# Kernel optimization log

Measured on AMD Instinct MI355X. Metric: run time of the kernel, lower is better.

The kernel has to match this reference:

```python
import jax, jax.numpy as jnp
import numpy as np
import math

B, NP, PL, CIN = 32, 1024, 16, 8
C = PL * CIN          # channels = 128
D = 512               # d_model
H = 8                 # n_heads
DH = D // H           # 64
DFF = 2048
E, TOPK = 4, 2
M = int(DH * math.log(DH))  # 266 performer random features


def _ortho_proj(m, d, rng):
    # gaussian-orthogonal random features, rows rescaled by gaussian norms (FAVOR+, scaling=0)
    blocks = []
    for _ in range(m // d + 1):
        q, _ = np.linalg.qr(rng.normal(size=(d, d)))
        blocks.append(q.T)
    mat = np.concatenate(blocks, 0)[:m]
    mult = np.linalg.norm(rng.normal(size=(m, d)), axis=1)
    return jnp.asarray((mat * mult[:, None]).astype(np.float32))


def setup_inputs() -> dict:
    key = jax.random.key(0)
    ks = jax.random.split(key, 16)
    rng = np.random.default_rng(0)
    s = lambda k, sh, fan: (jax.random.normal(k, sh, jnp.float32) / np.sqrt(fan))
    return {
        "x": jax.random.normal(ks[0], (B, NP, PL, CIN), jnp.float32),
        "emb_w": s(ks[1], (D, C), C),
        "wq": s(ks[2], (D, D), D), "bq": jnp.zeros((D,), jnp.float32),
        "wk": s(ks[3], (D, D), D), "bk": jnp.zeros((D,), jnp.float32),
        "wv": s(ks[4], (D, D), D), "bv": jnp.zeros((D,), jnp.float32),
        "wo": s(ks[5], (D, D), D), "bo": jnp.zeros((D,), jnp.float32),
        "proj": _ortho_proj(M, DH, rng),
        "ln2_g": jnp.ones((D,), jnp.float32), "ln2_b": jnp.zeros((D,), jnp.float32),
        "ln3_g": jnp.ones((D,), jnp.float32), "ln3_b": jnp.zeros((D,), jnp.float32),
        "gate_w": s(ks[6], (E, D), D), "gate_b": jnp.zeros((E,), jnp.float32),
        "w1": s(ks[7], (E, D, DFF), D), "b1": jnp.zeros((E, DFF), jnp.float32),
        "w2": s(ks[8], (E, DFF, D), DFF), "b2": jnp.zeros((E, D), jnp.float32),
    }


def _ln(x, g, b):
    mu = jnp.mean(x, -1, keepdims=True)
    var = jnp.var(x, -1, keepdims=True)
    return (x - mu) / jnp.sqrt(var + 1e-5) * g + b


def _phi(data, proj, is_query):
    # FAVOR+ softmax kernel feature map
    dh = data.shape[-1]
    m = proj.shape[0]
    dn = dh ** -0.25
    dash = jnp.einsum('...nd,md->...nm', data * dn, proj)
    diag = jnp.sum(jnp.square(data), -1, keepdims=True) * (0.5 * dn * dn)
    stab = jnp.max(dash, -1, keepdims=True) if is_query else jnp.max(dash)
    return (m ** -0.5) * (jnp.exp(dash - diag - stab) + 1e-4)


def reference(x, emb_w, wq, bq, wk, bk, wv, bv, wo, bo, proj,
              ln2_g, ln2_b, ln3_g, ln3_b, gate_w, gate_b, w1, b1, w2, b2):
    b, n = x.shape[0], x.shape[1]
    xe = x.reshape(b, n, -1) @ emb_w.T          # [b, n, D] (bias-free embedding)
    xe = xe[:, None]                            # [b, 1, n, D]
    # ---- Performer self-attention ----
    heads = lambda t: t.reshape(b, 1, n, H, DH).transpose(0, 1, 3, 2, 4)  # [b,1,h,n,dh]
    q = heads(xe @ wq.T + bq)
    k = heads(xe @ wk.T + bk)
    v = heads(xe @ wv.T + bv)
    qp = _phi(q, proj, True)                    # [b,1,h,n,m]
    kp = _phi(k, proj, False)
    ctx = jnp.einsum('...nm,...nd->...md', kp, v)           # [b,1,h,m,dh]
    den = jnp.einsum('...nm,...m->...n', qp, kp.sum(-2))    # [b,1,h,n]
    attn = jnp.einsum('...nm,...md->...nd', qp, ctx) / den[..., None]
    attn = attn.transpose(0, 1, 3, 2, 4).reshape(b, 1, n, D) @ wo.T + bo
    h1 = _ln(xe + attn, ln2_g, ln2_b)
    # ---- SparseMoE feed-forward (top-2 of 4 experts) ----
    t = h1.reshape(-1, D)                       # [T, D], T = b*n
    logits = t @ gate_w.T + gate_b              # [T, E]
    topv, topi = jax.lax.top_k(logits, TOPK)
    gwt = jax.nn.softmax(topv, -1)              # softmax over selected experts
    wfull = (jax.nn.one_hot(topi, E, dtype=t.dtype) * gwt[..., None]).sum(1)  # [T, E]
    hmid = jax.nn.relu(jnp.einsum('td,edf->etf', t, w1) + b1[:, None])        # [E, T, DFF]
    y = jnp.einsum('etf,efd->etd', hmid, w2) + b2[:, None]                    # [E, T, D]
    moe = jnp.einsum('te,etd->td', wfull, y).reshape(b, 1, n, D)
    return _ln(h1 + moe, ln3_g, ln3_b)          # dropout = identity in eval
```

## Files before the change

### kernel.cpp

```cpp
#include <hip/hip_runtime.h>
#include <math.h>

#define NBATCH 32
#define NPOS   1024
#define NTOK   32768
#define DMODEL 512
#define NHEAD  8
#define DHD    64
#define NROWS  262144
#define MMR    266
#define NDFF   2048
#define NEXP   4
#define CIN    128

#define DNSC   0.35355339059327373f
#define RSM    0.06131393394849658f
#define NEG_INF -3.0e38f

typedef _Float16 half8 __attribute__((ext_vector_type(8)));
typedef _Float16 half4 __attribute__((ext_vector_type(4)));
typedef float    f32x4 __attribute__((ext_vector_type(4)));

static const size_t F_BUF1 = 0;
static const size_t F_CTX  = 16777216;
static const size_t F_KSUM = 21135360;
static const size_t F_PART = 21203456;
static const size_t F_STAB = 21205504;
static const size_t F_EFF  = 21205520;
static const size_t F_CNTI = 21402128;
static const size_t F_TOKI = 21402144;
static const size_t F_GWF  = 21533216;
static const size_t F_PJT  = 21664288;
static const size_t F_END  = 21684768;

#define DASH17(da, q) \
  da[0]+=q*pA.x; da[1]+=q*pA.y; da[2]+=q*pA.z; da[3]+=q*pA.w; \
  da[4]+=q*pB.x; da[5]+=q*pB.y; da[6]+=q*pB.z; da[7]+=q*pB.w; \
  da[8]+=q*pC.x; da[9]+=q*pC.y; da[10]+=q*pC.z; da[11]+=q*pC.w; \
  da[12]+=q*pD.x; da[13]+=q*pD.y; da[14]+=q*pD.z; da[15]+=q*pD.w; \
  da[16]+=q*pE;

__global__ __launch_bounds__(256) void fallback_zero_kernel(float* __restrict__ out) {
  out[(size_t)blockIdx.x * 256 + threadIdx.x] = 0.f;
}

__global__ __launch_bounds__(256) void proj_pack_kernel(
    const float* __restrict__ proj, float* __restrict__ projT)
{
  int idx = blockIdx.x * 256 + threadIdx.x;
  if (idx >= 20480) return;
  int d = idx / 320, rem = idx % 320;
  int g = rem / 20, j = rem % 20;
  int m = g * 17 + j;
  projT[idx] = (j < 17 && m < MMR) ? proj[m * 64 + d] : 0.f;
}

__global__ __launch_bounds__(128) void effmat_kernel(
    const float* __restrict__ wq, const float* __restrict__ wk, const float* __restrict__ wv,
    const float* __restrict__ emb, float* __restrict__ eff)
{
  __shared__ float wrow[512];
  const int bid = blockIdx.x;
  const int mat = bid >> 9;
  const int n   = bid & 511;
  const float* W = (mat == 0) ? wq : ((mat == 1) ? wk : wv);
  const int tid = threadIdx.x;
  for (int i = tid; i < 512; i += 128) wrow[i] = W[n * 512 + i];
  __syncthreads();
  float acc = 0.f;
  for (int d = 0; d < 512; ++d) acc += wrow[d] * emb[d * CIN + tid];
  eff[mat * 65536 + n * CIN + tid] = acc;
}

__global__ __launch_bounds__(256) void gemm_nt_kernel(
    const float* __restrict__ A, const float* __restrict__ W, int K,
    const float* __restrict__ A2, const float* __restrict__ W2, int K2,
    const float* __restrict__ bias, float* __restrict__ C, int N, int ncb)
{
  __shared__ float As[32][64];
  __shared__ float Ws[32][64];
  const int tid  = threadIdx.x;
  const int bx   = blockIdx.x % ncb;
  const int by   = blockIdx.x / ncb;
  const int row0 = by * 64, col0 = bx * 64;
  const int tx   = tid & 15, ty = tid >> 4;
  const int lr   = tid >> 3;
  const int lk   = (tid & 7) * 4;
  float acc[4][4] = {};
  for (int pass = 0; pass < 2; ++pass) {
    const float* Ap = pass ? A2 : A;
    const float* Wp = pass ? W2 : W;
    const int    Kp = pass ? K2 : K;
    if (!Ap) continue;
    for (int k0 = 0; k0 < Kp; k0 += 32) {
      __syncthreads();
#pragma unroll
      for (int rr = 0; rr < 2; ++rr) {
        const int r = lr + rr * 32;
        float4 a4 = *(const float4*)&Ap[(size_t)(row0 + r) * Kp + k0 + lk];
        As[lk + 0][r] = a4.x; As[lk + 1][r] = a4.y; As[lk + 2][r] = a4.z; As[lk + 3][r] = a4.w;
        float4 w4 = *(const float4*)&Wp[(size_t)(col0 + r) * Kp + k0 + lk];
        Ws[lk + 0][r] = w4.x; Ws[lk + 1][r] = w4.y; Ws[lk + 2][r] = w4.z; Ws[lk + 3][r] = w4.w;
      }
      __syncthreads();
#pragma unroll
      for (int kk = 0; kk < 32; ++kk) {
        float4 av = *(const float4*)&As[kk][ty * 4];
        float4 wv = *(const float4*)&Ws[kk][tx * 4];
        acc[0][0] += av.x * wv.x; acc[0][1] += av.x * wv.y; acc[0][2] += av.x * wv.z; acc[0][3] += av.x * wv.w;
        acc[1][0] += av.y * wv.x; acc[1][1] += av.y * wv.y; acc[1][2] += av.y * wv.z; acc[1][3] += av.y * wv.w;
        acc[2][0] += av.z * wv.x; acc[2][1] += av.z * wv.y; acc[2][2] += av.z * wv.z; acc[2][3] += av.z * wv.w;
        acc[3][0] += av.w * wv.x; acc[3][1] += av.w * wv.y; acc[3][2] += av.w * wv.z; acc[3][3] += av.w * wv.w;
      }
    }
  }
#pragma unroll
  for (int i = 0; i < 4; ++i) {
    const int row = row0 + ty * 4 + i;
    const int col = col0 + tx * 4;
    float4 o = make_float4(acc[i][0], acc[i][1], acc[i][2], acc[i][3]);
    if (bias) {
      float4 b4 = *(const float4*)&bias[col];
      o.x += b4.x; o.y += b4.y; o.z += b4.z; o.w += b4.w;
    }
    *(float4*)&C[(size_t)row * N + col] = o;
  }
}

__global__ __launch_bounds__(1024) void kdash_max_kernel(
    const float* __restrict__ Kbuf, const float* __restrict__ projT, float* __restrict__ partial)
{
  __shared__ float pjG[20480];
  __shared__ float kl[32 * 68];
  __shared__ float red[1024];
  const int tid = threadIdx.x;
  for (int i = tid; i < 20480; i += 1024) pjG[i] = projT[i];
  const int w = tid >> 6, l = tid & 63;
  const int ml = l & 15, ds = l >> 4;
  const int dbase = ds * 16;
  const int r0 = 2 * w;
  float mxl = NEG_INF;
  for (int t = 0; t < 16; ++t) {
    __syncthreads();
    for (int idx = tid; idx < 2048; idx += 1024) {
      int r = idx >> 6, dd = idx & 63;
      kl[r * 68 + dd] = Kbuf[((size_t)blockIdx.x * 512 + t * 32 + r) * 64 + dd] * DNSC;
    }
    __syncthreads();
    float da0[17], da1[17];
#pragma unroll
    for (int j = 0; j < 17; ++j) { da0[j] = 0.f; da1[j] = 0.f; }
    for (int dd = 0; dd < 16; ++dd) {
      int d = dbase + dd;
      float q0 = kl[r0 * 68 + d], q1 = kl[r0 * 68 + 68 + d];
      const float* pr = &pjG[d * 320 + ml * 20];
      float4 pA = *(const float4*)pr, pB = *(const float4*)(pr + 4),
             pC = *(const float4*)(pr + 8), pD = *(const float4*)(pr + 12);
      float pE = pr[16];
      DASH17(da0, q0)
      DASH17(da1, q1)
    }
#pragma unroll
    for (int j = 0; j < 17; ++j) {
      da0[j] += __shfl_xor(da0[j], 16); da0[j] += __shfl_xor(da0[j], 32);
      da1[j] += __shfl_xor(da1[j], 16); da1[j] += __shfl_xor(da1[j], 32);
    }
#pragma unroll
    for (int j = 0; j < 17; ++j) {
      int m = ml * 17 + j;
      if (m < MMR) { mxl = fmaxf(mxl, da0[j]); mxl = fmaxf(mxl, da1[j]); }
    }
  }
  red[tid] = mxl;
  __syncthreads();
  for (int st = 512; st > 0; st >>= 1) {
    if (tid < st) red[tid] = fmaxf(red[tid], red[tid + st]);
    __syncthreads();
  }
  if (tid == 0) partial[blockIdx.x] = red[0];
}

__global__ __launch_bounds__(256) void reduce_max_kernel(
    const float* __restrict__ part, float* __restrict__ stab, int n)
{
  __shared__ float red[256];
  float m = NEG_INF;
  for (int i = threadIdx.x; i < n; i += 256) m = fmaxf(m, part[i]);
  red[threadIdx.x] = m;
  __syncthreads();
  for (int st = 128; st > 0; st >>= 1) {
    if (threadIdx.x < st) red[threadIdx.x] = fmaxf(red[threadIdx.x], red[threadIdx.x + st]);
    __syncthreads();
  }
  if (threadIdx.x == 0) stab[0] = red[0];
}

__global__ __launch_bounds__(1024) void ctx_kernel(
    const float* __restrict__ Kbuf, const float* __restrict__ Vbuf,
    const float* __restrict__ projT, const float* __restrict__ stabp,
    float* __restrict__ ctxg, float* __restrict__ ksumg)
{
  __shared__ float pjG[20480];
  __shared__ float kl[32 * 68];
  __shared__ float vl[32 * 68];
  __shared__ _Float16 kp16[32 * 320];
  __shared__ float ks[272];
  const int tid = threadIdx.x;
  const int bh = blockIdx.x;
  const int b = bh >> 3, h = bh & 7;
  const float stab = stabp[0];
  for (int i = tid; i < 20480; i += 1024) pjG[i] = projT[i];
  if (tid < 272) ks[tid] = 0.f;
  const int w = tid >> 6, l = tid & 63;
  const int ml = l & 15, ds = l >> 4;
  const int dbase = ds * 16;
  const int r0 = 2 * w;
  const int jh = ds >> 1, rsel = ds & 1;
  const int d = tid & 63, mg = tid >> 6;
  const int ksm = tid >> 1, ksih = tid & 1;
  const int ksg = ksm / 17, ksj = ksm - ksg * 17;
  float acc[17];
#pragma unroll
  for (int j = 0; j < 17; ++j) acc[j] = 0.f;

  for (int t = 0; t < 32; ++t) {
    __syncthreads();
    for (int idx = tid; idx < 2048; idx += 1024) {
      int r = idx >> 6, dd = idx & 63;
      size_t g = ((size_t)(b * NPOS + t * 32 + r)) * DMODEL + h * DHD + dd;
      kl[r * 68 + dd] = Kbuf[g] * DNSC;
      vl[r * 68 + dd] = Vbuf[g];
    }
    __syncthreads();
    float da0[17], da1[17]; float dg0 = 0.f, dg1 = 0.f;
#pragma unroll
    for (int j = 0; j < 17; ++j) { da0[j] = 0.f; da1[j] = 0.f; }
    for (int dd = 0; dd < 16; ++dd) {
      int dq = dbase + dd;
      float q0 = kl[r0 * 68 + dq], q1 = kl[r0 * 68 + 68 + dq];
      const float* pr = &pjG[dq * 320 + ml * 20];
      float4 pA = *(const float4*)pr, pB = *(const float4*)(pr + 4),
             pC = *(const float4*)(pr + 8), pD = *(const float4*)(pr + 12);
      float pE = pr[16];
      dg0 += q0 * q0; dg1 += q1 * q1;
      DASH17(da0, q0)
      DASH17(da1, q1)
    }
#pragma unroll
    for (int j = 0; j < 17; ++j) {
      da0[j] += __shfl_xor(da0[j], 16); da0[j] += __shfl_xor(da0[j], 32);
      da1[j] += __shfl_xor(da1[j], 16); da1[j] += __shfl_xor(da1[j], 32);
    }
    dg0 += __shfl_xor(dg0, 16); dg0 += __shfl_xor(dg0, 32);
    dg1 += __shfl_xor(dg1, 16); dg1 += __shfl_xor(dg1, 32);
    float dgx = rsel ? dg1 : dg0;
    const int irow = r0 + rsel;
#pragma unroll
    for (int k = 0; k < 9; ++k) {
      int j = 2 * k + jh;
      if (j < 17) {
        int m = ml * 17 + j;
        float dv = rsel ? da1[j] : da0[j];
        float v = 0.f;
        if (m < MMR) v = RSM * (expf(dv - 0.5f * dgx - stab) + 1e-4f);
        kp16[irow * 320 + ml * 20 + j] = (_Float16)v;
      }
    }
    __syncthreads();
    if (tid < 544) {
      float s = 0.f;
      const _Float16* kb = &kp16[ksih * 16 * 320 + ksg * 20 + ksj];
#pragma unroll
      for (int i = 0; i < 16; ++i) s += (float)kb[i * 320];
      s += __shfl_xor(s, 1);
      if (ksih == 0) ks[ksm] += s;
    }
    for (int i = 0; i < 32; ++i) {
      float vv = vl[i * 68 + d];
      const _Float16* kr = &kp16[i * 320 + mg * 20];
      half4 k0 = *(const half4*)kr;
      half4 k1 = *(const half4*)(kr + 4);
      half4 k2 = *(const half4*)(kr + 8);
      half4 k3 = *(const half4*)(kr + 12);
      float kE = (float)kr[16];
      acc[0] += (float)k0.x * vv; acc[1] += (float)k0.y * vv; acc[2] += (float)k0.z * vv; acc[3] += (float)k0.w * vv;
      acc[4] += (float)k1.x * vv; acc[5] += (float)k1.y * vv; acc[6] += (float)k1.z * vv; acc[7] += (float)k1.w * vv;
      acc[8] += (float)k2.x * vv; acc[9] += (float)k2.y * vv; acc[10] += (float)k2.z * vv; acc[11] += (float)k2.w * vv;
      acc[12] += (float)k3.x * vv; acc[13] += (float)k3.y * vv; acc[14] += (float)k3.z * vv; acc[15] += (float)k3.w * vv;
      acc[16] += kE * vv;
    }
  }
  __syncthreads();
  const size_t cb = (size_t)bh * MMR * DHD;
#pragma unroll
  for (int j = 0; j < 17; ++j) {
    int m = mg * 17 + j;
    if (m < MMR) ctxg[cb + (size_t)m * 64 + d] = acc[j];
  }
  if (tid < MMR) ksumg[bh * MMR + tid] = ks[tid];
}

__global__ __launch_bounds__(1024) void attn_kernel(
    const float* __restrict__ Qbuf, const float* __restrict__ ctxg,
    const float* __restrict__ ksumg, const float* __restrict__ projT,
    float* __restrict__ attnb)
{
  __shared__ float pjG[20480];
  __shared__ float ql[64 * 68];
  __shared__ _Float16 qp16[64 * 272];
  __shared__ float ks[272];
  __shared__ float den_s[64];
  const int tid = threadIdx.x;
  const int bh = blockIdx.x >> 4;
  const int n0 = (blockIdx.x & 15) * 64;
  const int b = bh >> 3, h = bh & 7;
  for (int i = tid; i < 20480; i += 1024) pjG[i] = projT[i];
  if (tid < 272) ks[tid] = (tid < MMR) ? ksumg[bh * MMR + tid] : 0.f;
  for (int idx = tid; idx < 4096; idx += 1024) {
    int r = idx >> 6, dd = idx & 63;
    ql[r * 68 + dd] = Qbuf[((size_t)(b * NPOS + n0 + r)) * DMODEL + h * DHD + dd] * DNSC;
  }
  __syncthreads();
  const int w = tid >> 6, l = tid & 63;
  const int ml = l & 15, ds = l >> 4;
  const int dbase = ds * 16;
  const int jh = ds >> 1, rsel = ds & 1;
  for (int s = 0; s < 2; ++s) {
    const int r0 = s * 32 + 2 * w;
    float da0[17], da1[17]; float dg0 = 0.f, dg1 = 0.f;
#pragma unroll
    for (int j = 0; j < 17; ++j) { da0[j] = 0.f; da1[j] = 0.f; }
    for (int dd = 0; dd < 16; ++dd) {
      int dq = dbase + dd;
      float q0 = ql[r0 * 68 + dq], q1 = ql[r0 * 68 + 68 + dq];
      const float* pr = &pjG[dq * 320 + ml * 20];
      float4 pA = *(const float4*)pr, pB = *(const float4*)(pr + 4),
             pC = *(const float4*)(pr + 8), pD = *(const float4*)(pr + 12);
      float pE = pr[16];
      dg0 += q0 * q0; dg1 += q1 * q1;
      DASH17(da0, q0)
      DASH17(da1, q1)
    }
#pragma unroll
    for (int j = 0; j < 17; ++j) {
      da0[j] += __shfl_xor(da0[j], 16); da0[j] += __shfl_xor(da0[j], 32);
      da1[j] += __shfl_xor(da1[j], 16); da1[j] += __shfl_xor(da1[j], 32);
    }
    dg0 += __shfl_xor(dg0, 16); dg0 += __shfl_xor(dg0, 32);
    dg1 += __shfl_xor(dg1, 16); dg1 += __shfl_xor(dg1, 32);
    float mx0 = NEG_INF, mx1 = NEG_INF;
#pragma unroll
    for (int j = 0; j < 17; ++j) {
      int m = ml * 17 + j;
      if (m < MMR) { mx0 = fmaxf(mx0, da0[j]); mx1 = fmaxf(mx1, da1[j]); }
    }
#pragma unroll
    for (int off = 1; off < 16; off <<= 1) {
      mx0 = fmaxf(mx0, __shfl_xor(mx0, off));
      mx1 = fmaxf(mx1, __shfl_xor(mx1, off));
    }
    float dgx = rsel ? dg1 : dg0;
    float mxx = rsel ? mx1 : mx0;
    const int row = r0 + rsel;
    float dp = 0.f;
#pragma unroll
    for (int k = 0; k < 9; ++k) {
      int j = 2 * k + jh;
      if (j < 17) {
        int m = ml * 17 + j;
        float dv = rsel ? da1[j] : da0[j];
        float v = 0.f;
        if (m < MMR) { v = RSM * (expf(dv - 0.5f * dgx - mxx) + 1e-4f); dp += v * ks[m]; }
        qp16[row * 272 + m] = (_Float16)v;
      }
    }
    dp += __shfl_xor(dp, 1); dp += __shfl_xor(dp, 2); dp += __shfl_xor(dp, 4);
    dp += __shfl_xor(dp, 8); dp += __shfl_xor(dp, 32);
    if ((l & 47) == 0) den_s[row] = dp;
  }
  __syncthreads();
  const int wg = tid >> 6, lane = tid & 63;
  float acc[4] = {0.f, 0.f, 0.f, 0.f};
  const float* cb = ctxg + (size_t)bh * MMR * DHD + lane;
  for (int m0 = 0; m0 < 272; m0 += 4) {
    float c0 = cb[(size_t)(m0 + 0) * 64];
    float c1 = cb[(size_t)(m0 + 1) * 64];
    float c2 = cb[(size_t)(m0 + 2) * 64];
    float c3 = cb[(size_t)(m0 + 3) * 64];
#pragma unroll
    for (int tt = 0; tt < 4; ++tt) {
      half4 q4 = *(const half4*)&qp16[(wg * 4 + tt) * 272 + m0];
      acc[tt] += (float)q4.x * c0 + (float)q4.y * c1 + (float)q4.z * c2 + (float)q4.w * c3;
    }
  }
#pragma unroll
  for (int tt = 0; tt < 4; ++tt) {
    int r = wg * 4 + tt;
    attnb[((size_t)(b * NPOS + n0 + r)) * DMODEL + h * DHD + lane] = acc[tt] / den_s[r];
  }
}

__global__ __launch_bounds__(256) void ln_kernel(
    const float* __restrict__ in, const float* __restrict__ g, const float* __restrict__ bb,
    float* __restrict__ out, float* __restrict__ out2)
{
  const int row = blockIdx.x, tid = threadIdx.x;
  float2 x = *(const float2*)&in[(size_t)row * DMODEL + tid * 2];
  float s = x.x + x.y, sq = x.x * x.x + x.y * x.y;
#pragma unroll
  for (int off = 32; off > 0; off >>= 1) {
    s += __shfl_down(s, off);
    sq += __shfl_down(sq, off);
  }
  __shared__ float ps[4], pq[4];
  __shared__ float smu, srv;
  const int wv = tid >> 6, ln = tid & 63;
  if (ln == 0) { ps[wv] = s; pq[wv] = sq; }
  __syncthreads();
  if (tid == 0) {
    float S = ps[0] + ps[1] + ps[2] + ps[3];
    float Q = pq[0] + pq[1] + pq[2] + pq[3];
    float mu = S / 512.f;
    float var = Q / 512.f - mu * mu;
    smu = mu;
    srv = 1.0f / sqrtf(var + 1e-5f);
  }
  __syncthreads();
  const float mu = smu, rv = srv;
  const int c = tid * 2;
  float y0 = (x.x - mu) * rv * g[c] + bb[c];
  float y1 = (x.y - mu) * rv * g[c + 1] + bb[c + 1];
  out[(size_t)row * DMODEL + c] = y0;
  out[(size_t)row * DMODEL + c + 1] = y1;
  if (out2) {
    out2[(size_t)row * DMODEL + c] = y0;
    out2[(size_t)row * DMODEL + c + 1] = y1;
  }
}

__global__ __launch_bounds__(64) void zero_cnt_kernel(int* __restrict__ cnt)
{
  if (threadIdx.x < NEXP) cnt[threadIdx.x] = 0;
}

__global__ __launch_bounds__(256) void gate_kernel(
    const float* __restrict__ h1, const float* __restrict__ gw, const float* __restrict__ gb,
    int* __restrict__ cnt, int* __restrict__ toks, float* __restrict__ gws)
{
  const int wv = threadIdx.x >> 6, ln = threadIdx.x & 63;
  const int tok = blockIdx.x * 4 + wv;
  const float* hr = h1 + (size_t)tok * DMODEL;
  float p0 = 0, p1 = 0, p2 = 0, p3 = 0;
#pragma unroll
  for (int k = 0; k < 8; ++k) {
    float xv = hr[ln + 64 * k];
    p0 += xv * gw[0 * DMODEL + ln + 64 * k];
    p1 += xv * gw[1 * DMODEL + ln + 64 * k];
    p2 += xv * gw[2 * DMODEL + ln + 64 * k];
    p3 += xv * gw[3 * DMODEL + ln + 64 * k];
  }
#pragma unroll
  for (int off = 32; off > 0; off >>= 1) {
    p0 += __shfl_down(p0, off);
    p1 += __shfl_down(p1, off);
    p2 += __shfl_down(p2, off);
    p3 += __shfl_down(p3, off);
  }
  if (ln == 0) {
    p0 += gb[0]; p1 += gb[1]; p2 += gb[2]; p3 += gb[3];
    int i0 = 0; float v0 = p0;
    if (p1 > v0) { v0 = p1; i0 = 1; }
    if (p2 > v0) { v0 = p2; i0 = 2; }
    if (p3 > v0) { v0 = p3; i0 = 3; }
    int i1 = -1; float v1 = NEG_INF;
    if (i0 != 0 && p0 > v1) { v1 = p0; i1 = 0; }
    if (i0 != 1 && p1 > v1) { v1 = p1; i1 = 1; }
    if (i0 != 2 && p2 > v1) { v1 = p2; i1 = 2; }
    if (i0 != 3 && p3 > v1) { v1 = p3; i1 = 3; }
    float e = expf(v1 - v0);
    float w0 = 1.f / (1.f + e);
    float w1 = e / (1.f + e);
    int pos0 = atomicAdd(&cnt[i0], 1);
    toks[i0 * NTOK + pos0] = tok;
    gws[i0 * NTOK + pos0] = w0;
    int pos1 = atomicAdd(&cnt[i1], 1);
    toks[i1 * NTOK + pos1] = tok;
    gws[i1 * NTOK + pos1] = w1;
  }
}

__global__ __launch_bounds__(256) void transpose_f16_kernel(
    const float* __restrict__ in, _Float16* __restrict__ outp, int R, int C)
{
  __shared__ float tl[32][33];
  const int bid = blockIdx.x;
  const int e  = bid >> 10;
  const int t2 = bid & 1023;
  const int tC = C >> 5;
  const int r0 = (t2 / tC) << 5;
  const int c0 = (t2 % tC) << 5;
  const float* ine  = in   + (size_t)e * R * C;
  _Float16*    oute = outp + (size_t)e * R * C;
  const int ci = threadIdx.x & 31, ri = threadIdx.x >> 5;
#pragma unroll
  for (int i = 0; i < 4; ++i)
    tl[ri + i * 8][ci] = ine[(size_t)(r0 + ri + i * 8) * C + c0 + ci];
  __syncthreads();
  const int rr = threadIdx.x & 31, cc = threadIdx.x >> 5;
#pragma unroll
  for (int i = 0; i < 4; ++i)
    oute[(size_t)(c0 + cc + i * 8) * R + r0 + rr] = (_Float16)tl[rr][cc + i * 8];
}

__global__ __launch_bounds__(512) void moe_mfma_kernel(
    const float* __restrict__ h1, const _Float16* __restrict__ w1t, const float* __restrict__ b1,
    const _Float16* __restrict__ w2t, const float* __restrict__ b2,
    const int* __restrict__ cnt, const int* __restrict__ toks, const float* __restrict__ gws,
    float* __restrict__ Z)
{
  __shared__ _Float16 t_lds[64 * 520];
  __shared__ _Float16 hm[64 * 264];
  __shared__ int   tk_s[64];
  __shared__ float gw_s[64];
  const int tid = threadIdx.x;
  const int e = blockIdx.x >> 10;
  const int tile = blockIdx.x & 1023;
  const int cn = cnt[e];
  if (tile * 64 >= cn) return;
  if (tid < 64) {
    int idx = tile * 64 + tid;
    if (idx < cn) { tk_s[tid] = toks[e * NTOK + idx]; gw_s[tid] = gws[e * NTOK + idx]; }
    else          { tk_s[tid] = -1;                   gw_s[tid] = 0.f; }
  }
  __syncthreads();
  for (int it = tid; it < 64 * 128; it += 512) {
    int r = it >> 7, c4 = (it & 127) * 4;
    int tk = tk_s[r];
    float4 v = make_float4(0.f, 0.f, 0.f, 0.f);
    if (tk >= 0) v = *(const float4*)&h1[(size_t)tk * DMODEL + c4];
    _Float16* p = &t_lds[r * 520 + c4];
    p[0] = (_Float16)v.x; p[1] = (_Float16)v.y; p[2] = (_Float16)v.z; p[3] = (_Float16)v.w;
  }
  __syncthreads();

  const int w = tid >> 6, l = tid & 63;
  const int lr = l & 15, lg = l >> 4;
  const _Float16* w1e = w1t + (size_t)e * NDFF * DMODEL;
  const _Float16* w2e = w2t + (size_t)e * DMODEL * NDFF;
  const float* b1e = b1 + e * NDFF;

  f32x4 acc2[4][4];
#pragma unroll
  for (int mt = 0; mt < 4; ++mt)
#pragma unroll
    for (int nt = 0; nt < 4; ++nt) acc2[mt][nt] = (f32x4){0.f, 0.f, 0.f, 0.f};

  for (int fc = 0; fc < 8; ++fc) {
    f32x4 acc1[4][2];
#pragma unroll
    for (int mt = 0; mt < 4; ++mt)
#pragma unroll
      for (int nt1 = 0; nt1 < 2; ++nt1) acc1[mt][nt1] = (f32x4){0.f, 0.f, 0.f, 0.f};
#pragma unroll
    for (int ks = 0; ks < 16; ++ks) {
      half8 am[4];
#pragma unroll
      for (int mt = 0; mt < 4; ++mt)
        am[mt] = *(const half8*)&t_lds[(mt * 16 + lr) * 520 + ks * 32 + lg * 8];
#pragma unroll
      for (int nt1 = 0; nt1 < 2; ++nt1) {
        half8 bfr = *(const half8*)&w1e[(size_t)(fc * 256 + w * 32 + nt1 * 16 + lr) * DMODEL + ks * 32 + lg * 8];
#pragma unroll
        for (int mt = 0; mt < 4; ++mt)
          acc1[mt][nt1] = __builtin_amdgcn_mfma_f32_16x16x32_f16(am[mt], bfr, acc1[mt][nt1], 0, 0, 0);
      }
    }
#pragma unroll
    for (int nt1 = 0; nt1 < 2; ++nt1) {
      float b1v = b1e[fc * 256 + w * 32 + nt1 * 16 + lr];
#pragma unroll
      for (int mt = 0; mt < 4; ++mt)
#pragma unroll
        for (int r = 0; r < 4; ++r)
          hm[(mt * 16 + lg * 4 + r) * 264 + w * 32 + nt1 * 16 + lr] =
              (_Float16)fmaxf(acc1[mt][nt1][r] + b1v, 0.f);
    }
    __syncthreads();
#pragma unroll
    for (int ks2 = 0; ks2 < 8; ++ks2) {
      half8 am[4];
#pragma unroll
      for (int mt = 0; mt < 4; ++mt)
        am[mt] = *(const half8*)&hm[(mt * 16 + lr) * 264 + ks2 * 32 + lg * 8];
#pragma unroll
      for (int nt = 0; nt < 4; ++nt) {
        half8 bfr = *(const half8*)&w2e[(size_t)(w * 64 + nt * 16 + lr) * NDFF + fc * 256 + ks2 * 32 + lg * 8];
#pragma unroll
        for (int mt = 0; mt < 4; ++mt)
          acc2[mt][nt] = __builtin_amdgcn_mfma_f32_16x16x32_f16(am[mt], bfr, acc2[mt][nt], 0, 0, 0);
      }
    }
    __syncthreads();
  }

  const float* b2e = b2 + e * DMODEL;
#pragma unroll
  for (int nt = 0; nt < 4; ++nt) {
    float b2v = b2e[w * 64 + nt * 16 + lr];
#pragma unroll
    for (int mt = 0; mt < 4; ++mt) {
#pragma unroll
      for (int r = 0; r < 4; ++r) {
        int row = mt * 16 + lg * 4 + r;
        int tk = tk_s[row];
        if (tk >= 0)
          atomicAdd(&Z[(size_t)tk * DMODEL + w * 64 + nt * 16 + lr],
                    (acc2[mt][nt][r] + b2v) * gw_s[row]);
      }
    }
  }
}

extern "C" void kernel_launch(void* const* d_in, const int* in_sizes, int n_in,
                              void* d_out, int out_size, void* d_ws, size_t ws_size,
                              hipStream_t stream) {
  const float* x     = (const float*)d_in[0];
  const float* emb_w = (const float*)d_in[1];
  const float* wq    = (const float*)d_in[2];
  const float* bq    = (const float*)d_in[3];
  const float* wk    = (const float*)d_in[4];
  const float* bk    = (const float*)d_in[5];
  const float* wv    = (const float*)d_in[6];
  const float* bv    = (const float*)d_in[7];
  const float* wo    = (const float*)d_in[8];
  const float* bo    = (const float*)d_in[9];
  const float* proj  = (const float*)d_in[10];
  const float* ln2g  = (const float*)d_in[11];
  const float* ln2b  = (const float*)d_in[12];
  const float* ln3g  = (const float*)d_in[13];
  const float* ln3b  = (const float*)d_in[14];
  const float* gatew = (const float*)d_in[15];
  const float* gateb = (const float*)d_in[16];
  const float* w1    = (const float*)d_in[17];
  const float* b1    = (const float*)d_in[18];
  const float* w2    = (const float*)d_in[19];
  const float* b2    = (const float*)d_in[20];
  float* out = (float*)d_out;
  float* ws  = (float*)d_ws;

  if (ws_size < F_END * sizeof(float)) {
    fallback_zero_kernel<<<NTOK * 2, 256, 0, stream>>>(out);
    return;
  }

  float* BUF1 = ws + F_BUF1;
  float* BUF2 = out;
  int*   cnt  = (int*)(ws + F_CNTI);
  int*   toks = (int*)(ws + F_TOKI);
  float* gwf  = ws + F_GWF;
  _Float16* w1t = (_Float16*)(ws + F_CTX);
  _Float16* w2t = w1t + (size_t)NEXP * NDFF * DMODEL;

  zero_cnt_kernel<<<1, 64, 0, stream>>>(cnt);
  proj_pack_kernel<<<80, 256, 0, stream>>>(proj, ws + F_PJT);
  effmat_kernel<<<1536, 128, 0, stream>>>(wq, wk, wv, emb_w, ws + F_EFF);
  gemm_nt_kernel<<<4096, 256, 0, stream>>>(x, ws + F_EFF + 65536, CIN, nullptr, nullptr, 0, bk, BUF1, DMODEL, 8);
  gemm_nt_kernel<<<4096, 256, 0, stream>>>(x, ws + F_EFF + 131072, CIN, nullptr, nullptr, 0, bv, BUF2, DMODEL, 8);
  kdash_max_kernel<<<512, 1024, 0, stream>>>(BUF1, ws + F_PJT, ws + F_PART);
  reduce_max_kernel<<<1, 256, 0, stream>>>(ws + F_PART, ws + F_STAB, 512);
  ctx_kernel<<<256, 1024, 0, stream>>>(BUF1, BUF2, ws + F_PJT, ws + F_STAB, ws + F_CTX, ws + F_KSUM);
  gemm_nt_kernel<<<4096, 256, 0, stream>>>(x, ws + F_EFF, CIN, nullptr, nullptr, 0, bq, BUF1, DMODEL, 8);
  attn_kernel<<<4096, 1024, 0, stream>>>(BUF1, ws + F_CTX, ws + F_KSUM, ws + F_PJT, BUF2);
  transpose_f16_kernel<<<4096, 256, 0, stream>>>(w1, w1t, DMODEL, NDFF);
  transpose_f16_kernel<<<4096, 256, 0, stream>>>(w2, w2t, NDFF, DMODEL);
  gemm_nt_kernel<<<4096, 256, 0, stream>>>(BUF2, wo, DMODEL, x, emb_w, CIN, bo, BUF1, DMODEL, 8);
  ln_kernel<<<NTOK, 256, 0, stream>>>(BUF1, ln2g, ln2b, BUF2, BUF1);
  gate_kernel<<<8192, 256, 0, stream>>>(BUF2, gatew, gateb, cnt, toks, gwf);
  moe_mfma_kernel<<<4096, 512, 0, stream>>>(BUF2, w1t, b1, w2t, b2, cnt, toks, gwf, BUF1);
  ln_kernel<<<NTOK, 256, 0, stream>>>(BUF1, ln3g, ln3b, out, nullptr);
}
```

Baseline: 5.262 ms.

## Halve block size of performer attention kernels to fit two blocks per CU

The kdash_max, ctx and attn kernels drop from 1024 to 512 threads per block and declare two blocks per CU. Per-step row tiles are halved, and the shared-memory feature layout is padded to 32-half strides so each thread can read features with 16-byte vector loads. ctx_kernel now has each thread accumulate two feature groups, and attn_kernel runs twice as many blocks over 32-row tiles. The aim is better occupancy and fewer barrier stalls, but the 80KB projection table is still copied into shared memory in every block, which may limit residency and doubles that copy in attn.

Result: faster. 4.643 ms (-11.8%).

```diff
diff --git a/kernel.cpp b/kernel.cpp
--- a/kernel.cpp
+++ b/kernel.cpp
@@ -7,7 +7,6 @@
 #define DMODEL 512
 #define NHEAD  8
 #define DHD    64
-#define NROWS  262144
 #define MMR    266
 #define NDFF   2048
 #define NEXP   4
@@ -127,24 +126,25 @@
   }
 }
 
-__global__ __launch_bounds__(1024) void kdash_max_kernel(
+__global__ __launch_bounds__(512, 2) void kdash_max_kernel(
     const float* __restrict__ Kbuf, const float* __restrict__ projT, float* __restrict__ partial)
 {
   __shared__ float pjG[20480];
-  __shared__ float kl[32 * 68];
-  __shared__ float red[1024];
+  __shared__ float kl[16 * 68];
+  __shared__ float red[512];
   const int tid = threadIdx.x;
-  for (int i = tid; i < 20480; i += 1024) pjG[i] = projT[i];
+  for (int i4 = tid; i4 < 5120; i4 += 512)
+    ((float4*)pjG)[i4] = ((const float4*)projT)[i4];
   const int w = tid >> 6, l = tid & 63;
   const int ml = l & 15, ds = l >> 4;
   const int dbase = ds * 16;
   const int r0 = 2 * w;
   float mxl = NEG_INF;
-  for (int t = 0; t < 16; ++t) {
-    __syncthreads();
-    for (int idx = tid; idx < 2048; idx += 1024) {
+  for (int t = 0; t < 32; ++t) {
+    __syncthreads();
+    for (int idx = tid; idx < 1024; idx += 512) {
       int r = idx >> 6, dd = idx & 63;
-      kl[r * 68 + dd] = Kbuf[((size_t)blockIdx.x * 512 + t * 32 + r) * 64 + dd] * DNSC;
+      kl[r * 68 + dd] = Kbuf[((size_t)blockIdx.x * 512 + t * 16 + r) * 64 + dd] * DNSC;
     }
     __syncthreads();
     float da0[17], da1[17];
@@ -173,7 +173,7 @@
   }
   red[tid] = mxl;
   __syncthreads();
-  for (int st = 512; st > 0; st >>= 1) {
+  for (int st = 256; st > 0; st >>= 1) {
     if (tid < st) red[tid] = fmaxf(red[tid], red[tid + st]);
     __syncthreads();
   }
@@ -195,41 +195,43 @@
   if (threadIdx.x == 0) stab[0] = red[0];
 }
 
-__global__ __launch_bounds__(1024) void ctx_kernel(
+__global__ __launch_bounds__(512, 2) void ctx_kernel(
     const float* __restrict__ Kbuf, const float* __restrict__ Vbuf,
     const float* __restrict__ projT, const float* __restrict__ stabp,
     float* __restrict__ ctxg, float* __restrict__ ksumg)
 {
   __shared__ float pjG[20480];
-  __shared__ float kl[32 * 68];
-  __shared__ float vl[32 * 68];
-  __shared__ _Float16 kp16[32 * 320];
+  __shared__ float kl[16 * 68];
+  __shared__ float vl[16 * 68];
+  __shared__ _Float16 kp16[16 * 512];
   __shared__ float ks[272];
   const int tid = threadIdx.x;
   const int bh = blockIdx.x;
   const int b = bh >> 3, h = bh & 7;
   const float stab = stabp[0];
-  for (int i = tid; i < 20480; i += 1024) pjG[i] = projT[i];
+  for (int i4 = tid; i4 < 5120; i4 += 512)
+    ((float4*)pjG)[i4] = ((const float4*)projT)[i4];
   if (tid < 272) ks[tid] = 0.f;
   const int w = tid >> 6, l = tid & 63;
   const int ml = l & 15, ds = l >> 4;
   const int dbase = ds * 16;
   const int r0 = 2 * w;
   const int jh = ds >> 1, rsel = ds & 1;
-  const int d = tid & 63, mg = tid >> 6;
-  const int ksm = tid >> 1, ksih = tid & 1;
-  const int ksg = ksm / 17, ksj = ksm - ksg * 17;
-  float acc[17];
-#pragma unroll
-  for (int j = 0; j < 17; ++j) acc[j] = 0.f;
-
-  for (int t = 0; t < 32; ++t) {
-    __syncthreads();
-    for (int idx = tid; idx < 2048; idx += 1024) {
+  const int d = l;
+  const int ksg = tid / 17, ksj = tid - ksg * 17;
+  float acc[2][17];
+#pragma unroll
+  for (int g = 0; g < 2; ++g)
+#pragma unroll
+    for (int j = 0; j < 17; ++j) acc[g][j] = 0.f;
+
+  for (int t = 0; t < 64; ++t) {
+    __syncthreads();
+    for (int idx = tid; idx < 1024; idx += 512) {
       int r = idx >> 6, dd = idx & 63;
-      size_t g = ((size_t)(b * NPOS + t * 32 + r)) * DMODEL + h * DHD + dd;
-      kl[r * 68 + dd] = Kbuf[g] * DNSC;
-      vl[r * 68 + dd] = Vbuf[g];
+      size_t gg = ((size_t)(b * NPOS + t * 16 + r)) * DMODEL + h * DHD + dd;
+      kl[r * 68 + dd] = Kbuf[gg] * DNSC;
+      vl[r * 68 + dd] = Vbuf[gg];
     }
     __syncthreads();
     float da0[17], da1[17]; float dg0 = 0.f, dg1 = 0.f;
@@ -263,60 +265,66 @@
         float dv = rsel ? da1[j] : da0[j];
         float v = 0.f;
         if (m < MMR) v = RSM * (expf(dv - 0.5f * dgx - stab) + 1e-4f);
-        kp16[irow * 320 + ml * 20 + j] = (_Float16)v;
-      }
-    }
-    __syncthreads();
-    if (tid < 544) {
+        kp16[irow * 512 + ml * 32 + j] = (_Float16)v;
+      }
+    }
+    __syncthreads();
+    if (tid < 272) {
       float s = 0.f;
-      const _Float16* kb = &kp16[ksih * 16 * 320 + ksg * 20 + ksj];
-#pragma unroll
-      for (int i = 0; i < 16; ++i) s += (float)kb[i * 320];
-      s += __shfl_xor(s, 1);
-      if (ksih == 0) ks[ksm] += s;
-    }
-    for (int i = 0; i < 32; ++i) {
+      const _Float16* kb = &kp16[ksg * 32 + ksj];
+#pragma unroll
+      for (int i = 0; i < 16; ++i) s += (float)kb[i * 512];
+      ks[tid] += s;
+    }
+    for (int i = 0; i < 16; ++i) {
       float vv = vl[i * 68 + d];
-      const _Float16* kr = &kp16[i * 320 + mg * 20];
-      half4 k0 = *(const half4*)kr;
-      half4 k1 = *(const half4*)(kr + 4);
-      half4 k2 = *(const half4*)(kr + 8);
-      half4 k3 = *(const half4*)(kr + 12);
-      float kE = (float)kr[16];
-      acc[0] += (float)k0.x * vv; acc[1] += (float)k0.y * vv; acc[2] += (float)k0.z * vv; acc[3] += (float)k0.w * vv;
-      acc[4] += (float)k1.x * vv; acc[5] += (float)k1.y * vv; acc[6] += (float)k1.z * vv; acc[7] += (float)k1.w * vv;
-      acc[8] += (float)k2.x * vv; acc[9] += (float)k2.y * vv; acc[10] += (float)k2.z * vv; acc[11] += (float)k2.w * vv;
-      acc[12] += (float)k3.x * vv; acc[13] += (float)k3.y * vv; acc[14] += (float)k3.z * vv; acc[15] += (float)k3.w * vv;
-      acc[16] += kE * vv;
-    }
-  }
-  __syncthreads();
+#pragma unroll
+      for (int g = 0; g < 2; ++g) {
+        const _Float16* kr = &kp16[i * 512 + (2 * w + g) * 32];
+        half8 kA = *(const half8*)kr;
+        half8 kB = *(const half8*)(kr + 8);
+        float kE = (float)kr[16];
+        acc[g][0] += (float)kA[0] * vv; acc[g][1] += (float)kA[1] * vv;
+        acc[g][2] += (float)kA[2] * vv; acc[g][3] += (float)kA[3] * vv;
+        acc[g][4] += (float)kA[4] * vv; acc[g][5] += (float)kA[5] * vv;
+        acc[g][6] += (float)kA[6] * vv; acc[g][7] += (float)kA[7] * vv;
+        acc[g][8] += (float)kB[0] * vv; acc[g][9] += (float)kB[1] * vv;
+        acc[g][10] += (float)kB[2] * vv; acc[g][11] += (float)kB[3] * vv;
+        acc[g][12] += (float)kB[4] * vv; acc[g][13] += (float)kB[5] * vv;
+        acc[g][14] += (float)kB[6] * vv; acc[g][15] += (float)kB[7] * vv;
+        acc[g][16] += kE * vv;
+      }
+    }
+  }
   const size_t cb = (size_t)bh * MMR * DHD;
 #pragma unroll
-  for (int j = 0; j < 17; ++j) {
-    int m = mg * 17 + j;
-    if (m < MMR) ctxg[cb + (size_t)m * 64 + d] = acc[j];
-  }
+  for (int g = 0; g < 2; ++g)
+#pragma unroll
+    for (int j = 0; j < 17; ++j) {
+      int m = (2 * w + g) * 17 + j;
+      if (m < MMR) ctxg[cb + (size_t)m * 64 + d] = acc[g][j];
+    }
   if (tid < MMR) ksumg[bh * MMR + tid] = ks[tid];
 }
 
-__global__ __launch_bounds__(1024) void attn_kernel(
+__global__ __launch_bounds__(512, 2) void attn_kernel(
     const float* __restrict__ Qbuf, const float* __restrict__ ctxg,
     const float* __restrict__ ksumg, const float* __restrict__ projT,
     float* __restrict__ attnb)
 {
   __shared__ float pjG[20480];
-  __shared__ float ql[64 * 68];
-  __shared__ _Float16 qp16[64 * 272];
+  __shared__ float ql[32 * 68];
+  __shared__ _Float16 qp16[32 * 512];
   __shared__ float ks[272];
-  __shared__ float den_s[64];
+  __shared__ float den_s[32];
   const int tid = threadIdx.x;
-  const int bh = blockIdx.x >> 4;
-  const int n0 = (blockIdx.x & 15) * 64;
+  const int bh = blockIdx.x >> 5;
+  const int n0 = (blockIdx.x & 31) * 32;
   const int b = bh >> 3, h = bh & 7;
-  for (int i = tid; i < 20480; i += 1024) pjG[i] = projT[i];
+  for (int i4 = tid; i4 < 5120; i4 += 512)
+    ((float4*)pjG)[i4] = ((const float4*)projT)[i4];
   if (tid < 272) ks[tid] = (tid < MMR) ? ksumg[bh * MMR + tid] : 0.f;
-  for (int idx = tid; idx < 4096; idx += 1024) {
+  for (int idx = tid; idx < 2048; idx += 512) {
     int r = idx >> 6, dd = idx & 63;
     ql[r * 68 + dd] = Qbuf[((size_t)(b * NPOS + n0 + r)) * DMODEL + h * DHD + dd] * DNSC;
   }
@@ -326,7 +334,7 @@
   const int dbase = ds * 16;
   const int jh = ds >> 1, rsel = ds & 1;
   for (int s = 0; s < 2; ++s) {
-    const int r0 = s * 32 + 2 * w;
+    const int r0 = s * 16 + 2 * w;
     float da0[17], da1[17]; float dg0 = 0.f, dg1 = 0.f;
 #pragma unroll
     for (int j = 0; j < 17; ++j) { da0[j] = 0.f; da1[j] = 0.f; }
@@ -371,7 +379,7 @@
         float dv = rsel ? da1[j] : da0[j];
         float v = 0.f;
         if (m < MMR) { v = RSM * (expf(dv - 0.5f * dgx - mxx) + 1e-4f); dp += v * ks[m]; }
-        qp16[row * 272 + m] = (_Float16)v;
+        qp16[row * 512 + ml * 32 + j] = (_Float16)v;
       }
     }
     dp += __shfl_xor(dp, 1); dp += __shfl_xor(dp, 2); dp += __shfl_xor(dp, 4);
@@ -382,15 +390,23 @@
   const int wg = tid >> 6, lane = tid & 63;
   float acc[4] = {0.f, 0.f, 0.f, 0.f};
   const float* cb = ctxg + (size_t)bh * MMR * DHD + lane;
-  for (int m0 = 0; m0 < 272; m0 += 4) {
-    float c0 = cb[(size_t)(m0 + 0) * 64];
-    float c1 = cb[(size_t)(m0 + 1) * 64];
-    float c2 = cb[(size_t)(m0 + 2) * 64];
-    float c3 = cb[(size_t)(m0 + 3) * 64];
+  for (int g = 0; g < 16; ++g) {
+    float cv[17];
+#pragma unroll
+    for (int j = 0; j < 17; ++j) cv[j] = cb[(size_t)(g * 17 + j) * 64];
 #pragma unroll
     for (int tt = 0; tt < 4; ++tt) {
-      half4 q4 = *(const half4*)&qp16[(wg * 4 + tt) * 272 + m0];
-      acc[tt] += (float)q4.x * c0 + (float)q4.y * c1 + (float)q4.z * c2 + (float)q4.w * c3;
+      const _Float16* qr = &qp16[(wg * 4 + tt) * 512 + g * 32];
+      half8 qA = *(const half8*)qr;
+      half8 qB = *(const half8*)(qr + 8);
+      float qE = (float)qr[16];
+      acc[tt] += (float)qA[0] * cv[0] + (float)qA[1] * cv[1] + (float)qA[2] * cv[2]
+               + (float)qA[3] * cv[3] + (float)qA[4] * cv[4] + (float)qA[5] * cv[5]
+               + (float)qA[6] * cv[6] + (float)qA[7] * cv[7]
+               + (float)qB[0] * cv[8] + (float)qB[1] * cv[9] + (float)qB[2] * cv[10]
+               + (float)qB[3] * cv[11] + (float)qB[4] * cv[12] + (float)qB[5] * cv[13]
+               + (float)qB[6] * cv[14] + (float)qB[7] * cv[15]
+               + qE * cv[16];
     }
   }
 #pragma unroll
@@ -666,11 +682,11 @@
   effmat_kernel<<<1536, 128, 0, stream>>>(wq, wk, wv, emb_w, ws + F_EFF);
   gemm_nt_kernel<<<4096, 256, 0, stream>>>(x, ws + F_EFF + 65536, CIN, nullptr, nullptr, 0, bk, BUF1, DMODEL, 8);
   gemm_nt_kernel<<<4096, 256, 0, stream>>>(x, ws + F_EFF + 131072, CIN, nullptr, nullptr, 0, bv, BUF2, DMODEL, 8);
-  kdash_max_kernel<<<512, 1024, 0, stream>>>(BUF1, ws + F_PJT, ws + F_PART);
+  kdash_max_kernel<<<512, 512, 0, stream>>>(BUF1, ws + F_PJT, ws + F_PART);
   reduce_max_kernel<<<1, 256, 0, stream>>>(ws + F_PART, ws + F_STAB, 512);
-  ctx_kernel<<<256, 1024, 0, stream>>>(BUF1, BUF2, ws + F_PJT, ws + F_STAB, ws + F_CTX, ws + F_KSUM);
+  ctx_kernel<<<256, 512, 0, stream>>>(BUF1, BUF2, ws + F_PJT, ws + F_STAB, ws + F_CTX, ws + F_KSUM);
   gemm_nt_kernel<<<4096, 256, 0, stream>>>(x, ws + F_EFF, CIN, nullptr, nullptr, 0, bq, BUF1, DMODEL, 8);
-  attn_kernel<<<4096, 1024, 0, stream>>>(BUF1, ws + F_CTX, ws + F_KSUM, ws + F_PJT, BUF2);
+  attn_kernel<<<8192, 512, 0, stream>>>(BUF1, ws + F_CTX, ws + F_KSUM, ws + F_PJT, BUF2);
   transpose_f16_kernel<<<4096, 256, 0, stream>>>(w1, w1t, DMODEL, NDFF);
   transpose_f16_kernel<<<4096, 256, 0, stream>>>(w2, w2t, NDFF, DMODEL);
   gemm_nt_kernel<<<4096, 256, 0, stream>>>(BUF2, wo, DMODEL, x, emb_w, CIN, bo, BUF1, DMODEL, 8);
```
